# Kernel optimization log

Measured on AMD Instinct MI355X. Metric: run time of the kernel, lower is better.

Reference implementation:

```python
import jax, jax.numpy as jnp
import numpy as np

ENC_DIM, DEC_DIM, HID_DIM = 512, 1024, 128
B, T = 64, 2048


def setup_inputs() -> dict:
    key = jax.random.key(0)
    ks = jax.random.split(key, 8)
    encoder_outs = jax.random.normal(ks[0], (B, T, ENC_DIM), dtype=jnp.float32)
    decoder_state = jax.random.normal(ks[1], (B, DEC_DIM), dtype=jnp.float32)
    mask = jax.random.randint(ks[2], (B, T), 0, 2) == 1
    # parameters (torch nn.Linear: y = x @ W.T + b)
    sV = 1.0 / np.sqrt(ENC_DIM)
    sW = 1.0 / np.sqrt(DEC_DIM)
    sw = 1.0 / np.sqrt(HID_DIM)
    V_w = jax.random.uniform(ks[3], (HID_DIM, ENC_DIM), minval=-sV, maxval=sV)
    V_b = jax.random.uniform(ks[4], (HID_DIM,), minval=-sV, maxval=sV)
    W_w = jax.random.uniform(ks[5], (HID_DIM, DEC_DIM), minval=-sW, maxval=sW)
    w_w = jax.random.uniform(ks[6], (1, HID_DIM), minval=-sw, maxval=sw)
    w_b = jax.random.uniform(ks[7], (1,), minval=-sw, maxval=sw)
    return {"encoder_outs": encoder_outs, "decoder_state": decoder_state,
            "mask": mask, "V_w": V_w, "V_b": V_b, "W_w": W_w,
            "w_w": w_w, "w_b": w_b}


def reference(encoder_outs, decoder_state, mask, V_w, V_b, W_w, w_w, w_b):
    # [B,1,H] query projection + [B,T,H] key projection
    q = jnp.einsum('bd,hd->bh', decoder_state, W_w)[:, None, :]
    k = jnp.einsum('bte,he->bth', encoder_outs, V_w) + V_b
    # scores: [B,T]
    erg = jnp.einsum('bth,h->bt', jnp.tanh(q + k), w_w[0]) + w_b[0]
    erg = jnp.where(mask, -jnp.inf, erg)
    attention_weights = jax.nn.softmax(erg, axis=1)
    attention_context = jnp.einsum('bte,bt->be', encoder_outs, attention_weights)
    return (attention_context, attention_weights)
```

## Files before the change

kernel.cpp:

```cpp
#include <hip/hip_runtime.h>
#include <hip/hip_bf16.h>

#define Bn   64
#define Tn   2048
#define ENCD 512
#define DECD 1024
#define HIDD 128
#define TT   32
#define NCH  (Tn / TT)
#define LROW 520

typedef __attribute__((ext_vector_type(8))) short bf16x8;
typedef __attribute__((ext_vector_type(4))) float f32x4;

__device__ __forceinline__ unsigned short f2bf(float f) {
    union { float f; unsigned u; } v; v.f = f;
    unsigned r = v.u + 0x7FFFu + ((v.u >> 16) & 1u);
    return (unsigned short)(r >> 16);
}
__device__ __forceinline__ float bf2f(unsigned short s) {
    union { unsigned u; float f; } v; v.u = ((unsigned)s) << 16;
    return v.f;
}
__device__ __forceinline__ float tanh_fast(float x) {
    float xa = fminf(fmaxf(x, -10.f), 10.f);
    float e = __expf(2.f * xa);
    return (e - 1.f) / (e + 1.f);
}

__global__ __launch_bounds__(256) void prep(
    const float* __restrict__ dec, const float* __restrict__ Ww,
    const float* __restrict__ Vb,  const float* __restrict__ Vw,
    float* __restrict__ qb, unsigned short* __restrict__ Vbf)
{
    const int blk = blockIdx.x, tid = threadIdx.x;
    if (blk < 512) {
        const int b = blk >> 3, hg = blk & 7;
        const int h_local = tid >> 4, seg = tid & 15;
        const int h = hg * 16 + h_local;
        const float* w = Ww + (size_t)h * DECD;
        const float* d = dec + (size_t)b * DECD;
        float acc = 0.f;
        #pragma unroll
        for (int j = 0; j < 16; ++j) {
            int f4 = j * 16 + seg;
            f32x4 a = *(const f32x4*)(d + f4 * 4);
            f32x4 bb = *(const f32x4*)(w + f4 * 4);
            acc += a.x * bb.x + a.y * bb.y + a.z * bb.z + a.w * bb.w;
        }
        acc += __shfl_xor(acc, 1);
        acc += __shfl_xor(acc, 2);
        acc += __shfl_xor(acc, 4);
        acc += __shfl_xor(acc, 8);
        if (seg == 0) qb[b * HIDD + h] = acc + Vb[h];
    } else {
        const int c = blk - 512;
        int f4 = c * 256 + tid;
        f32x4 v = *(const f32x4*)(Vw + f4 * 4);
        ushort4 u;
        u.x = f2bf(v.x); u.y = f2bf(v.y); u.z = f2bf(v.z); u.w = f2bf(v.w);
        *(ushort4*)&Vbf[f4 * 4] = u;
    }
}

__global__ __launch_bounds__(512, 8) void attn_main(
    const float* __restrict__ enc, const int* __restrict__ mask,
    const float* __restrict__ qb,  const unsigned short* __restrict__ Vbf,
    const float* __restrict__ ww,  const float* __restrict__ wb,
    float* __restrict__ pW, float* __restrict__ lC, float* __restrict__ ctxP)
{
    __shared__ unsigned short encS[TT * LROW];
    __shared__ float wpart[4][TT];

    const int chunk = blockIdx.x, b = blockIdx.y;
    const int tid = threadIdx.x;
    const int t0 = chunk * TT;
    const int wave = tid >> 6, lane = tid & 63;
    const int li = lane & 15, quad = lane >> 4;
    const int mg = wave & 1, ng = wave >> 1;

    const int h0 = ng * 32 + li;
    const int h1 = h0 + 16;
    const float qv0 = qb[b * HIDD + h0], qv1 = qb[b * HIDD + h1];
    const float wv0 = ww[h0],            wv1 = ww[h1];
    const float wbv = wb[0];
    const int mk = (lane < TT) ? mask[b * Tn + t0 + lane] : 1;

    const float* src = enc + ((size_t)b * Tn + t0) * ENCD;
    #pragma unroll
    for (int batch = 0; batch < 2; ++batch) {
        f32x4 v[4];
        #pragma unroll
        for (int j = 0; j < 4; ++j)
            v[j] = *(const f32x4*)(src + ((batch * 4 + j) * 512 + tid) * 4);
        #pragma unroll
        for (int j = 0; j < 4; ++j) {
            int f4 = (batch * 4 + j) * 512 + tid;
            int t = f4 >> 7, e = (f4 & 127) * 4;
            ushort4 u;
            u.x = f2bf(v[j].x); u.y = f2bf(v[j].y);
            u.z = f2bf(v[j].z); u.w = f2bf(v[j].w);
            *(ushort4*)&encS[t * LROW + e] = u;
        }
    }
    __syncthreads();

    f32x4 acc0 = (f32x4){0.f, 0.f, 0.f, 0.f};
    f32x4 acc1 = (f32x4){0.f, 0.f, 0.f, 0.f};
    const unsigned short* vrow0 = Vbf + (size_t)h0 * ENCD;
    const unsigned short* vrow1 = Vbf + (size_t)h1 * ENCD;
    const unsigned short* arow  = &encS[(mg * 16 + li) * LROW];

    #pragma unroll 4
    for (int ks = 0; ks < 16; ++ks) {
        int k0 = ks * 32 + quad * 8;
        bf16x8 a  = *(const bf16x8*)(arow + k0);
        bf16x8 b0 = *(const bf16x8*)(vrow0 + k0);
        bf16x8 b1 = *(const bf16x8*)(vrow1 + k0);
        acc0 = __builtin_amdgcn_mfma_f32_16x16x32_bf16(a, b0, acc0, 0, 0, 0);
        acc1 = __builtin_amdgcn_mfma_f32_16x16x32_bf16(a, b1, acc1, 0, 0, 0);
    }

    #pragma unroll
    for (int r = 0; r < 4; ++r) {
        float s = tanh_fast(acc0[r] + qv0) * wv0
                + tanh_fast(acc1[r] + qv1) * wv1;
        s += __shfl_xor(s, 1);
        s += __shfl_xor(s, 2);
        s += __shfl_xor(s, 4);
        s += __shfl_xor(s, 8);
        if (li == 0) wpart[ng][mg * 16 + quad * 4 + r] = s;
    }
    __syncthreads();

    float p = 0.f;
    if (lane < TT) {
        float v = wbv + wpart[0][lane] + wpart[1][lane]
                      + wpart[2][lane] + wpart[3][lane];
        p = (mk != 0) ? 0.f : __expf(v);
    }

    if (wave == 0) {
        float l = p;
        #pragma unroll
        for (int off = 32; off >= 1; off >>= 1)
            l += __shfl_xor(l, off);
        if (lane < TT) pW[(size_t)b * Tn + t0 + lane] = p;
        if (lane == 0) lC[b * NCH + chunk] = l;
    }

    {
        float c = 0.f;
        #pragma unroll
        for (int t = 0; t < TT; ++t) {
            float pt = __shfl(p, t);
            c += pt * bf2f(encS[t * LROW + tid]);
        }
        __builtin_nontemporal_store(c, &ctxP[((size_t)(b * NCH + chunk)) * ENCD + tid]);
    }
}

__global__ __launch_bounds__(256) void finalize(
    const float* __restrict__ lC, const float* __restrict__ pW,
    const float* __restrict__ ctxP, float* __restrict__ out)
{
    __shared__ float invLs;
    __shared__ float red[256];
    const int b = blockIdx.x, part = blockIdx.y, tid = threadIdx.x;
    const int wave = tid >> 6, lane = tid & 63;

    if (wave == 0) {
        float l = lC[b * NCH + lane];
        #pragma unroll
        for (int off = 32; off >= 1; off >>= 1)
            l += __shfl_xor(l, off);
        if (lane == 0) invLs = 1.f / l;
    }
    __syncthreads();
    const float invL = invLs;

    if (part < 4) {
        const int e = part * 128 + (tid & 127);
        const int half = tid >> 7;
        float c = 0.f;
        #pragma unroll 8
        for (int cc = half * 32; cc < half * 32 + 32; ++cc)
            c += ctxP[((size_t)(b * NCH + cc)) * ENCD + e];
        red[tid] = c;
        __syncthreads();
        if (tid < 128) {
            int ee = part * 128 + tid;
            out[b * ENCD + ee] = (red[tid] + red[tid + 128]) * invL;
        }
    } else {
        float* outw = out + Bn * ENCD;
        #pragma unroll
        for (int i = 0; i < 8; ++i) {
            int t = i * 256 + tid;
            outw[(size_t)b * Tn + t] = pW[(size_t)b * Tn + t] * invL;
        }
    }
}

extern "C" void kernel_launch(void* const* d_in, const int* in_sizes, int n_in,
                              void* d_out, int out_size, void* d_ws, size_t ws_size,
                              hipStream_t stream)
{
    const float* enc  = (const float*)d_in[0];
    const float* dec  = (const float*)d_in[1];
    const int*   mask = (const int*)d_in[2];
    const float* Vw   = (const float*)d_in[3];
    const float* Vb   = (const float*)d_in[4];
    const float* Ww   = (const float*)d_in[5];
    const float* ww   = (const float*)d_in[6];
    const float* wb   = (const float*)d_in[7];
    float* out = (float*)d_out;
    float* ws  = (float*)d_ws;

    float*          qb   = ws;
    unsigned short* Vbf  = (unsigned short*)(ws + 8192);
    float*          pW   = ws + 40960;
    float*          lC   = ws + 172032;
    float*          ctxP = ws + 180224;

    hipLaunchKernelGGL(prep, dim3(576), dim3(256), 0, stream, dec, Ww, Vb, Vw, qb, Vbf);
    hipLaunchKernelGGL(attn_main, dim3(NCH, Bn), dim3(512), 0, stream,
                       enc, mask, qb, Vbf, ww, wb, pW, lC, ctxP);
    hipLaunchKernelGGL(finalize, dim3(Bn, 5), dim3(256), 0, stream, lC, pW, ctxP, out);
}
```

Baseline: 446.8 us.

## Process four chunks per block with register prefetch of next encoder tile

Each attn_main block now loops over four consecutive 32-row chunks instead of one, with the grid shrunk by four. While the current chunk's MFMA, tanh scoring and context accumulation run, the next chunk's fp32 encoder tile is loaded into registers, overlapping global loads with compute. The change adds a barrier per chunk and raises register pressure (launch bounds lowered to 6), which reduces occupancy and the number of blocks available to hide latency.

Result: slower. 513.3 us (+14.9%).

```diff
diff --git a/kernel.cpp b/kernel.cpp
--- a/kernel.cpp
+++ b/kernel.cpp
@@ -8,6 +8,8 @@
 #define HIDD 128
 #define TT   32
 #define NCH  (Tn / TT)
+#define GRP  4
+#define NGB  (NCH / GRP)
 #define LROW 520
 
 typedef __attribute__((ext_vector_type(8))) short bf16x8;
@@ -63,7 +65,7 @@
     }
 }
 
-__global__ __launch_bounds__(512, 8) void attn_main(
+__global__ __launch_bounds__(512, 6) void attn_main(
     const float* __restrict__ enc, const int* __restrict__ mask,
     const float* __restrict__ qb,  const unsigned short* __restrict__ Vbf,
     const float* __restrict__ ww,  const float* __restrict__ wb,
@@ -72,91 +74,100 @@
     __shared__ unsigned short encS[TT * LROW];
     __shared__ float wpart[4][TT];
 
-    const int chunk = blockIdx.x, b = blockIdx.y;
+    const int g = blockIdx.x, b = blockIdx.y;
     const int tid = threadIdx.x;
-    const int t0 = chunk * TT;
     const int wave = tid >> 6, lane = tid & 63;
     const int li = lane & 15, quad = lane >> 4;
     const int mg = wave & 1, ng = wave >> 1;
-
-    const int h0 = ng * 32 + li;
-    const int h1 = h0 + 16;
+    const int c0 = g * GRP;
+
+    const int h0 = ng * 32 + li, h1 = h0 + 16;
     const float qv0 = qb[b * HIDD + h0], qv1 = qb[b * HIDD + h1];
     const float wv0 = ww[h0],            wv1 = ww[h1];
     const float wbv = wb[0];
-    const int mk = (lane < TT) ? mask[b * Tn + t0 + lane] : 1;
-
-    const float* src = enc + ((size_t)b * Tn + t0) * ENCD;
+    int mk[GRP];
     #pragma unroll
-    for (int batch = 0; batch < 2; ++batch) {
-        f32x4 v[4];
-        #pragma unroll
-        for (int j = 0; j < 4; ++j)
-            v[j] = *(const f32x4*)(src + ((batch * 4 + j) * 512 + tid) * 4);
-        #pragma unroll
-        for (int j = 0; j < 4; ++j) {
-            int f4 = (batch * 4 + j) * 512 + tid;
+    for (int c = 0; c < GRP; ++c)
+        mk[c] = (lane < TT) ? mask[b * Tn + (c0 + c) * TT + lane] : 1;
+
+    const float* srcBase = enc + ((size_t)b * Tn + c0 * TT) * ENCD;
+    const unsigned short* vrow0 = Vbf + (size_t)h0 * ENCD;
+    const unsigned short* vrow1 = Vbf + (size_t)h1 * ENCD;
+    const unsigned short* arow  = &encS[(mg * 16 + li) * LROW];
+
+    f32x4 v[8];
+    #pragma unroll
+    for (int j = 0; j < 8; ++j)
+        v[j] = *(const f32x4*)(srcBase + (j * 512 + tid) * 4);
+
+    for (int c = 0; c < GRP; ++c) {
+        #pragma unroll
+        for (int j = 0; j < 8; ++j) {
+            int f4 = j * 512 + tid;
             int t = f4 >> 7, e = (f4 & 127) * 4;
             ushort4 u;
             u.x = f2bf(v[j].x); u.y = f2bf(v[j].y);
             u.z = f2bf(v[j].z); u.w = f2bf(v[j].w);
             *(ushort4*)&encS[t * LROW + e] = u;
         }
-    }
-    __syncthreads();
-
-    f32x4 acc0 = (f32x4){0.f, 0.f, 0.f, 0.f};
-    f32x4 acc1 = (f32x4){0.f, 0.f, 0.f, 0.f};
-    const unsigned short* vrow0 = Vbf + (size_t)h0 * ENCD;
-    const unsigned short* vrow1 = Vbf + (size_t)h1 * ENCD;
-    const unsigned short* arow  = &encS[(mg * 16 + li) * LROW];
-
-    #pragma unroll 4
-    for (int ks = 0; ks < 16; ++ks) {
-        int k0 = ks * 32 + quad * 8;
-        bf16x8 a  = *(const bf16x8*)(arow + k0);
-        bf16x8 b0 = *(const bf16x8*)(vrow0 + k0);
-        bf16x8 b1 = *(const bf16x8*)(vrow1 + k0);
-        acc0 = __builtin_amdgcn_mfma_f32_16x16x32_bf16(a, b0, acc0, 0, 0, 0);
-        acc1 = __builtin_amdgcn_mfma_f32_16x16x32_bf16(a, b1, acc1, 0, 0, 0);
-    }
-
-    #pragma unroll
-    for (int r = 0; r < 4; ++r) {
-        float s = tanh_fast(acc0[r] + qv0) * wv0
-                + tanh_fast(acc1[r] + qv1) * wv1;
-        s += __shfl_xor(s, 1);
-        s += __shfl_xor(s, 2);
-        s += __shfl_xor(s, 4);
-        s += __shfl_xor(s, 8);
-        if (li == 0) wpart[ng][mg * 16 + quad * 4 + r] = s;
-    }
-    __syncthreads();
-
-    float p = 0.f;
-    if (lane < TT) {
-        float v = wbv + wpart[0][lane] + wpart[1][lane]
-                      + wpart[2][lane] + wpart[3][lane];
-        p = (mk != 0) ? 0.f : __expf(v);
-    }
-
-    if (wave == 0) {
-        float l = p;
-        #pragma unroll
-        for (int off = 32; off >= 1; off >>= 1)
-            l += __shfl_xor(l, off);
-        if (lane < TT) pW[(size_t)b * Tn + t0 + lane] = p;
-        if (lane == 0) lC[b * NCH + chunk] = l;
-    }
-
-    {
-        float c = 0.f;
-        #pragma unroll
-        for (int t = 0; t < TT; ++t) {
-            float pt = __shfl(p, t);
-            c += pt * bf2f(encS[t * LROW + tid]);
-        }
-        __builtin_nontemporal_store(c, &ctxP[((size_t)(b * NCH + chunk)) * ENCD + tid]);
+        __syncthreads();
+
+        if (c + 1 < GRP) {
+            const float* s2 = srcBase + (size_t)(c + 1) * TT * ENCD;
+            #pragma unroll
+            for (int j = 0; j < 8; ++j)
+                v[j] = *(const f32x4*)(s2 + (j * 512 + tid) * 4);
+        }
+
+        f32x4 acc0 = (f32x4){0.f, 0.f, 0.f, 0.f};
+        f32x4 acc1 = (f32x4){0.f, 0.f, 0.f, 0.f};
+        #pragma unroll 4
+        for (int ks = 0; ks < 16; ++ks) {
+            int k0 = ks * 32 + quad * 8;
+            bf16x8 a  = *(const bf16x8*)(arow + k0);
+            bf16x8 b0 = *(const bf16x8*)(vrow0 + k0);
+            bf16x8 b1 = *(const bf16x8*)(vrow1 + k0);
+            acc0 = __builtin_amdgcn_mfma_f32_16x16x32_bf16(a, b0, acc0, 0, 0, 0);
+            acc1 = __builtin_amdgcn_mfma_f32_16x16x32_bf16(a, b1, acc1, 0, 0, 0);
+        }
+
+        #pragma unroll
+        for (int r = 0; r < 4; ++r) {
+            float s = tanh_fast(acc0[r] + qv0) * wv0
+                    + tanh_fast(acc1[r] + qv1) * wv1;
+            s += __shfl_xor(s, 1);
+            s += __shfl_xor(s, 2);
+            s += __shfl_xor(s, 4);
+            s += __shfl_xor(s, 8);
+            if (li == 0) wpart[ng][mg * 16 + quad * 4 + r] = s;
+        }
+        __syncthreads();
+
+        float p = 0.f;
+        if (lane < TT) {
+            float vv = wbv + wpart[0][lane] + wpart[1][lane]
+                           + wpart[2][lane] + wpart[3][lane];
+            p = (mk[c] != 0) ? 0.f : __expf(vv);
+        }
+
+        if (wave == 0) {
+            float l = p;
+            #pragma unroll
+            for (int off = 32; off >= 1; off >>= 1)
+                l += __shfl_xor(l, off);
+            if (lane < TT) pW[(size_t)b * Tn + (c0 + c) * TT + lane] = p;
+            if (lane == 0) lC[b * NCH + c0 + c] = l;
+        }
+
+        {
+            float cx = 0.f;
+            #pragma unroll
+            for (int t = 0; t < TT; ++t)
+                cx += __shfl(p, t) * bf2f(encS[t * LROW + tid]);
+            __builtin_nontemporal_store(
+                cx, &ctxP[((size_t)(b * NCH + c0 + c)) * ENCD + tid]);
+        }
+        __syncthreads();
     }
 }
 
@@ -224,7 +235,7 @@
     float*          ctxP = ws + 180224;
 
     hipLaunchKernelGGL(prep, dim3(576), dim3(256), 0, stream, dec, Ww, Vb, Vw, qb, Vbf);
-    hipLaunchKernelGGL(attn_main, dim3(NCH, Bn), dim3(512), 0, stream,
+    hipLaunchKernelGGL(attn_main, dim3(NGB, Bn), dim3(512), 0, stream,
                        enc, mask, qb, Vbf, ww, wb, pW, lC, ctxP);
     hipLaunchKernelGGL(finalize, dim3(Bn, 5), dim3(256), 0, stream, lC, pW, ctxP, out);
 }
```
